# Optimization experiments

Hardware: AMD Instinct MI355X
Metric: run time of the kernel (lower is better)

The kernel has to match this reference:

```python
import jax, jax.numpy as jnp
import numpy as np

# Dims (see shape_source): resolution H must equal H_sp, W_sp must be 1 for the
# module's reshapes/broadcasts to be consistent.
B, HRES, WRES = 2, 4, 8192
H_SP, W_SP, H_SEC = 4, 1, 4          # window height, window width, sector height
C, NH = 512, 8
HD = C // NH
L = HRES * WRES                       # 32768 query tokens
NS = H_SEC * WRES                     # sector tokens (from k.view(B,C,H,W))
NW = B * (HRES // H_SP) * (WRES // W_SP)  # number of windows = B*WRES
SCALE = HD ** -0.5
EPS = 1e-5


def setup_inputs() -> dict:
    key = jax.random.key(0)
    ks = jax.random.split(key, 12)
    f32 = jnp.float32
    rn = lambda k, shp, s=1.0: jax.random.normal(k, shp, dtype=f32) * s
    return {
        "s": rn(ks[0], (B, NS, C)),
        "x": rn(ks[1], (B, L, C)),
        "s_pos": rn(ks[2], (B, H_SEC * W_SP, WRES // W_SP, 2)),
        "x_pos": rn(ks[3], (B, L, 2)),
        "Wq": rn(ks[4], (C, C), 0.02), "bq": jnp.zeros((C,), f32),
        "Wk": rn(ks[5], (C, C), 0.02), "bk": jnp.zeros((C,), f32),
        "Wv": rn(ks[6], (C, C), 0.02), "bv": jnp.zeros((C,), f32),
        "pw1": rn(ks[7], (16, 2), 0.3), "pb1": jnp.zeros((16,), f32),
        "bn_g": jnp.ones((16,), f32), "bn_b": jnp.zeros((16,), f32),
        "bn_m": jnp.zeros((16,), f32), "bn_v": jnp.ones((16,), f32),
        "pw2": rn(ks[8], (NH, 16), 0.3), "pb2": jnp.zeros((NH,), f32),
    }


def reference(s, x, s_pos, x_pos, Wq, bq, Wk, bk, Wv, bv,
              pw1, pb1, bn_g, bn_b, bn_m, bn_v, pw2, pb2):
    # ---- relative position bias (pointwise conv1d + BN(eval) + ReLU + conv1d) ----
    xp = x_pos.reshape(B, HRES // H_SP, H_SP, WRES // W_SP, W_SP, 2)
    xp = jnp.transpose(xp, (0, 1, 3, 5, 2, 4)).reshape(-1, 2, H_SP * W_SP)   # [NW,2,4]
    sp = jnp.transpose(s_pos, (0, 2, 3, 1)).reshape(-1, 2, H_SEC * W_SP)      # [NW,2,4]
    rel = xp[:, :, :, None] - sp[:, :, None, :]                               # [NW,2,4,4]
    rel = rel.reshape(NW, 2, -1)                                              # [NW,2,16]
    h = jnp.einsum('oc,ncl->nol', pw1, rel) + pb1[None, :, None]
    h = (h - bn_m[None, :, None]) * jax.lax.rsqrt(bn_v[None, :, None] + EPS)
    h = h * bn_g[None, :, None] + bn_b[None, :, None]
    h = jax.nn.relu(h)
    bias = jnp.einsum('oc,ncl->nol', pw2, h) + pb2[None, :, None]
    bias = bias.reshape(NW, NH, H_SP * W_SP, H_SEC * W_SP)                    # [NW,NH,4,4]

    # ---- q: im2cswin (true transpose to [B,C,H,W], then window partition) ----
    q = x @ Wq + bq                                                           # [B,L,C]
    q = jnp.transpose(q, (0, 2, 1)).reshape(B, C, HRES // H_SP, H_SP, WRES // W_SP, W_SP)
    q = jnp.transpose(q, (0, 2, 4, 3, 5, 1)).reshape(NW, H_SP * W_SP, NH, HD)
    q = jnp.transpose(q, (0, 2, 1, 3))                                        # [NW,NH,4,HD]

    # ---- k,v: raw view(B,C,H_sec,W) as in torch (memory reinterp, NOT transpose) ----
    def sector_windows(t):
        t = t.reshape(B, C, H_SEC, WRES)
        t = t.reshape(B, NH, HD, H_SEC, WRES // W_SP, W_SP)
        t = jnp.transpose(t, (0, 4, 1, 3, 5, 2))                              # [B,W,NH,Hs,Wsp,HD]
        return t.reshape(NW, NH, H_SEC * W_SP, HD)
    k = sector_windows(s @ Wk + bk)
    v = sector_windows(s @ Wv + bv)

    # ---- windowed attention with bias ----
    attn = jnp.einsum('nhqd,nhkd->nhqk', q * SCALE, k) + bias
    attn = jax.nn.softmax(attn, axis=-1)
    o = jnp.einsum('nhqk,nhkd->nhqd', attn, v)
    o = jnp.transpose(o, (0, 2, 1, 3)).reshape(NW, H_SP * W_SP, C)

    # ---- windows2img ----
    o = o.reshape(B, HRES // H_SP, WRES // W_SP, H_SP, W_SP, C)
    o = jnp.transpose(o, (0, 1, 3, 2, 4, 5)).reshape(B, L, C)
    return o
```

## Files before the change

kernel.cpp:

```cpp
#include <hip/hip_runtime.h>


typedef unsigned short u16;
typedef unsigned int u32;
typedef __attribute__((ext_vector_type(8))) short bf16x8;
typedef __attribute__((ext_vector_type(4))) float f32x4;
typedef __attribute__((ext_vector_type(8))) unsigned short u16x8;
typedef __attribute__((ext_vector_type(4))) unsigned short u16x4;
typedef __attribute__((ext_vector_type(4))) unsigned int u32x4;

__device__ __forceinline__ u16 f2b(float f) {
  u32 u = __float_as_uint(f);
  return (u16)((u + 0x7FFFu + ((u >> 16) & 1u)) >> 16);
}
__device__ __forceinline__ float b2f(u16 v) { return __uint_as_float(((u32)v) << 16); }
__device__ __forceinline__ float b2f_lo(u32 d) { return __uint_as_float(d << 16); }
__device__ __forceinline__ float b2f_hi(u32 d) { return __uint_as_float(d & 0xffff0000u); }
__device__ __forceinline__ u32 cvt_pk(float lo, float hi) {
  u32 r;
  asm("v_cvt_pk_bf16_f32 %0, %1, %2" : "=v"(r) : "v"(lo), "v"(hi));
  return r;
}
#define GLDS(g, l)                                                                     \
  __builtin_amdgcn_global_load_lds((const __attribute__((address_space(1))) void*)(g), \
                                   (__attribute__((address_space(3))) void*)(l), 16, 0, 0)
#define SBAR() __builtin_amdgcn_sched_barrier(0)

__global__ __launch_bounds__(256) void prep_kernel(
    const float* __restrict__ Wq, const float* __restrict__ Wk, const float* __restrict__ Wv,
    u16* __restrict__ Wt, const float* __restrict__ s, u16* __restrict__ sb,
    const float* __restrict__ xpos, const float* __restrict__ spos,
    const float* __restrict__ pw1, const float* __restrict__ pb1,
    const float* __restrict__ bng, const float* __restrict__ bnb,
    const float* __restrict__ bnm, const float* __restrict__ bnv,
    const float* __restrict__ pw2, const float* __restrict__ pb2, float* __restrict__ biasw) {
  int bid = (int)blockIdx.x;
  int t = threadIdx.x;
  if (bid < 16384) {
    size_t i = ((size_t)bid * 256 + t) * 8;
    float4 v0 = *(const float4*)(s + i);
    float4 v1 = *(const float4*)(s + i + 4);
    u32x4 pk;
    pk[0] = cvt_pk(v0.x, v0.y);
    pk[1] = cvt_pk(v0.z, v0.w);
    pk[2] = cvt_pk(v1.x, v1.y);
    pk[3] = cvt_pk(v1.z, v1.w);
    *(u32x4*)(sb + i) = pk;
  } else if (bid < 19456) {
    int r = bid - 16384;
    int mat = r >> 10, bx = r & 1023;
    const float* W = (mat == 0) ? Wq : (mat == 1) ? Wk : Wv;
    int g = bx * 256 + t;
    int n = g >> 9, k = g & 511;
    Wt[(size_t)mat * 262144 + g] = f2b(W[k * 512 + n]);
  } else {
    int bx = bid - 19456;
    int wl = t & 63, p = t >> 6;
    int n = bx * 64 + wl;
    int b = n >> 13, w = n & 8191;
    float Am[16], Bm[16], Cm[16];
#pragma unroll
    for (int m = 0; m < 16; ++m) {
      float scv = bng[m] * rsqrtf(bnv[m] + 1e-5f);
      Am[m] = pw1[2 * m] * scv;
      Bm[m] = pw1[2 * m + 1] * scv;
      Cm[m] = (pb1[m] - bnm[m]) * scv + bnb[m];
    }
    size_t xi = ((size_t)(b * 32768 + p * 8192 + w)) * 2;
    float xp0 = xpos[xi], xp1 = xpos[xi + 1];
#pragma unroll
    for (int ks = 0; ks < 4; ++ks) {
      size_t si = ((size_t)((b * 4 + ks) * 8192 + w)) * 2;
      float r0 = xp0 - spos[si];
      float r1 = xp1 - spos[si + 1];
      float o[8];
#pragma unroll
      for (int oo = 0; oo < 8; ++oo) o[oo] = pb2[oo];
#pragma unroll
      for (int m = 0; m < 16; ++m) {
        float h = fmaxf(Am[m] * r0 + Bm[m] * r1 + Cm[m], 0.f);
#pragma unroll
        for (int oo = 0; oo < 8; ++oo) o[oo] += pw2[oo * 16 + m] * h;
      }
#pragma unroll
      for (int oo = 0; oo < 8; ++oo)
        biasw[((size_t)(((b * 8 + oo) * 4 + p) * 4 + ks)) * 8192 + w] = o[oo];
    }
  }
}

__global__ __launch_bounds__(256, 3) void gemm_kernel(const float* __restrict__ A,
                                                      const u16* __restrict__ Bt,
                                                      const float* __restrict__ biasv,
                                                      u16* __restrict__ Out) {
  __shared__ u16 lds[24576];
  const int t = threadIdx.x, lane = t & 63, wv = t >> 6;
  const int id = (int)blockIdx.x;
  const int lg = (id & 7) * 256 + (id >> 3);
  const int mt = (lg >> 2) * 128, nt = (lg & 3) * 128;
  const int fr = lane & 15, kg = lane >> 4;
  const int wm = (wv & 1) * 64, wn = (wv >> 1) * 64;

  const int arow = lane >> 3;
  const int agr = (lane & 7) ^ arow;
  const int brow = lane >> 2;
  const int bgr = (lane & 3) ^ (brow & 3) ^ ((brow >> 2) & 3);

  const float* Abase = A + (size_t)mt * 512;
  const u16* Bbase = Bt + (size_t)nt * 512;

  f32x4 acc[4][4];
#pragma unroll
  for (int i = 0; i < 4; ++i)
#pragma unroll
    for (int j = 0; j < 4; ++j) acc[i][j] = (f32x4){0.f, 0.f, 0.f, 0.f};

#define STAGEQ(buf, kt)                                                       \
  {                                                                           \
    u16* Ab_ = lds + (buf)*8192;                                              \
    u16* Bb_ = lds + 16384 + (buf)*4096;                                      \
    _Pragma("unroll") for (int ii = 0; ii < 4; ++ii) {                        \
      int inst = wv * 4 + ii;                                                 \
      GLDS(Abase + (size_t)(inst * 8 + arow) * 512 + (kt) + agr * 4,          \
           Ab_ + inst * 512);                                                 \
    }                                                                         \
    _Pragma("unroll") for (int ii = 0; ii < 2; ++ii) {                        \
      int inst = wv * 2 + ii;                                                 \
      GLDS(Bbase + (size_t)(inst * 16 + brow) * 512 + (kt) + bgr * 8,         \
           Bb_ + inst * 512);                                                 \
    }                                                                         \
  }

  STAGEQ(0, 0);

  for (int ki = 0; ki < 16; ++ki) {
    int cur = ki & 1;
    if (ki < 15) {
      STAGEQ(cur ^ 1, (ki + 1) * 32);
      asm volatile("s_waitcnt vmcnt(6)" ::: "memory");
    } else {
      asm volatile("s_waitcnt vmcnt(0)" ::: "memory");
    }
    SBAR();
    __builtin_amdgcn_s_barrier();
    SBAR();

    const u16* Ab = lds + cur * 8192;
    const u16* Bb = lds + 16384 + cur * 4096;
    bf16x8 af[4], bfr[4];
#pragma unroll
    for (int i = 0; i < 4; ++i) {
      int r = wm + i * 16 + fr;
      int p0 = (2 * kg) ^ (r & 7), p1 = p0 ^ 1;
      f32x4 a0 = *(const f32x4*)&Ab[r * 64 + p0 * 8];
      f32x4 a1 = *(const f32x4*)&Ab[r * 64 + p1 * 8];
      union { bf16x8 v; u32 w[4]; } uu;
      uu.w[0] = cvt_pk(a0[0], a0[1]);
      uu.w[1] = cvt_pk(a0[2], a0[3]);
      uu.w[2] = cvt_pk(a1[0], a1[1]);
      uu.w[3] = cvt_pk(a1[2], a1[3]);
      af[i] = uu.v;
    }
#pragma unroll
    for (int j = 0; j < 4; ++j) {
      int r = wn + j * 16 + fr;
      int pos = kg ^ (r & 3) ^ ((r >> 2) & 3);
      bfr[j] = *(const bf16x8*)&Bb[r * 32 + pos * 8];
    }
    __builtin_amdgcn_s_setprio(1);
#pragma unroll
    for (int i = 0; i < 4; ++i)
#pragma unroll
      for (int j = 0; j < 4; ++j)
        acc[i][j] = __builtin_amdgcn_mfma_f32_16x16x32_bf16(af[i], bfr[j], acc[i][j], 0, 0, 0);
    __builtin_amdgcn_s_setprio(0);

    SBAR();
    __builtin_amdgcn_s_barrier();
    SBAR();
  }
#undef STAGEQ

  u16* Clds = lds;
#pragma unroll
  for (int i = 0; i < 4; ++i)
#pragma unroll
    for (int r = 0; r < 4; ++r) {
      int row = wm + i * 16 + kg * 4 + r;
#pragma unroll
      for (int j = 0; j < 4; ++j) {
        int ch = wn + j * 16 + fr;
        Clds[row * 136 + ch] = f2b(acc[i][j][r] + biasv[nt + ch]);
      }
    }
  __syncthreads();
#pragma unroll
  for (int c = 0; c < 8; ++c) {
    int off = c * 2048 + t * 8;
    int row = off >> 7, col = off & 127;
    *(u16x8*)(Out + (size_t)(mt + row) * 512 + nt + col) = *(const u16x8*)&Clds[row * 136 + col];
  }
}

__global__ __launch_bounds__(512, 4) void fused_attn_kernel(
    const u16* __restrict__ sb, const u16* __restrict__ WtK, const u16* __restrict__ WtV,
    const float* __restrict__ bK, const float* __restrict__ bV,
    const u16* __restrict__ Qt, const float* __restrict__ biasw, float* __restrict__ out) {
  __shared__ __align__(16) char LDS[74752];
  float* Xf = (float*)LDS;
  float* alds = (float*)(LDS + 4096);
  u16* Klds = (u16*)(LDS + 8192);
  u16* Vlds = (u16*)(LDS + 40960);

  const int t = threadIdx.x, lane = t & 63, wv = t >> 6;
  const int i0 = (int)blockIdx.x;
  const int xcd = i0 & 7, qq = i0 >> 3;
  const int g = (qq >> 6) * 8 + xcd, inner = qq & 63;
  const int b = g >> 4, u = g & 15;
  const int cg = inner >> 3, nh = inner & 7;
  const int fr = lane & 15, kg = lane >> 4;
  const int p3p = wv >> 1, dh = wv & 1;

  f32x4 accK[2][4], accV[2][4];
#pragma unroll
  for (int i = 0; i < 2; ++i)
#pragma unroll
    for (int j = 0; j < 4; ++j) {
      accK[i][j] = (f32x4){0.f, 0.f, 0.f, 0.f};
      accV[i][j] = (f32x4){0.f, 0.f, 0.f, 0.f};
    }

  const int lgr = (lane & 3) ^ ((lane >> 3) & 3);

#define STAGEF(buf, kt)                                                                 \
  {                                                                                     \
    u16* Sb_ = (u16*)(LDS) + (buf)*8192;                                                \
    _Pragma("unroll") for (int ii = 0; ii < 2; ++ii) {                                  \
      int i = wv * 2 + ii;                                                              \
      int r = i * 16 + (lane >> 2);                                                     \
      int grow = nh * 4096 + (r >> 2) * 64 + (r & 3) * 16 + u;                          \
      GLDS(sb + (size_t)(b * 32768 + grow) * 512 + (kt) + lgr * 8, Sb_ + i * 512);      \
    }                                                                                   \
    {                                                                                   \
      const u16* wsrc = (wv < 4) ? WtK : WtV;                                           \
      u16* Wb_ = (u16*)(LDS + 49152 + (buf)*8192 + ((wv < 4) ? 0 : 4096));              \
      int i = wv & 3;                                                                   \
      int r = i * 16 + (lane >> 2);                                                     \
      GLDS(wsrc + (size_t)(cg * 64 + r) * 512 + (kt) + lgr * 8, Wb_ + i * 512);         \
    }                                                                                   \
  }

  STAGEF(0, 0);
  STAGEF(1, 32);

  for (int ki = 0; ki < 16; ++ki) {
    int cur = ki % 3;
    if (ki < 15) {
      asm volatile("s_waitcnt vmcnt(3)" ::: "memory");
    } else {
      asm volatile("s_waitcnt vmcnt(0)" ::: "memory");
    }
    SBAR();
    __builtin_amdgcn_s_barrier();
    SBAR();

    const u16* Sb = (const u16*)(LDS) + cur * 8192;
    const u16* Kb = (const u16*)(LDS + 49152 + cur * 8192);
    const u16* Vb = (const u16*)(LDS + 49152 + cur * 8192 + 4096);
    bf16x8 af[2];
#pragma unroll
    for (int i = 0; i < 2; ++i) {
      int r = wv * 32 + i * 16 + fr;
      int gpos = kg ^ ((fr >> 1) & 3);
      af[i] = *(const bf16x8*)&Sb[r * 32 + gpos * 8];
    }
    {
      bf16x8 bkf[4];
#pragma unroll
      for (int j = 0; j < 4; ++j) {
        int r = j * 16 + fr;
        int gpos = kg ^ ((fr >> 1) & 3);
        bkf[j] = *(const bf16x8*)&Kb[r * 32 + gpos * 8];
      }
      __builtin_amdgcn_s_setprio(1);
#pragma unroll
      for (int i = 0; i < 2; ++i)
#pragma unroll
        for (int j = 0; j < 4; ++j)
          accK[i][j] = __builtin_amdgcn_mfma_f32_16x16x32_bf16(af[i], bkf[j], accK[i][j], 0, 0, 0);
      __builtin_amdgcn_s_setprio(0);
    }
    {
      bf16x8 bvf[4];
#pragma unroll
      for (int j = 0; j < 4; ++j) {
        int r = j * 16 + fr;
        int gpos = kg ^ ((fr >> 1) & 3);
        bvf[j] = *(const bf16x8*)&Vb[r * 32 + gpos * 8];
      }
      __builtin_amdgcn_s_setprio(1);
#pragma unroll
      for (int i = 0; i < 2; ++i)
#pragma unroll
        for (int j = 0; j < 4; ++j)
          accV[i][j] = __builtin_amdgcn_mfma_f32_16x16x32_bf16(af[i], bvf[j], accV[i][j], 0, 0, 0);
      __builtin_amdgcn_s_setprio(0);
    }
    SBAR();
    if (ki < 14) STAGEF((ki + 2) % 3, (ki + 2) * 32);
    SBAR();
  }
#undef STAGEF

  SBAR();
  float bkr[4], bvr[4];
#pragma unroll
  for (int j = 0; j < 4; ++j) {
    bkr[j] = bK[cg * 64 + j * 16 + fr];
    bvr[j] = bV[cg * 64 + j * 16 + fr];
  }
  u32x4 qv[4];
  {
    const u16* qp =
        Qt + (size_t)(b * 32768 + p3p * 8192 + u * 512 + cg * 64 + lane) * 512 + nh * 64 + dh * 32;
#pragma unroll
    for (int i = 0; i < 4; ++i) qv[i] = *(const u32x4*)(qp + i * 8);
  }
  float br[4];
  {
    const size_t bb = ((size_t)((b * 8 + nh) * 16 + p3p * 4)) * 8192 + u * 512 + cg * 64 + lane;
#pragma unroll
    for (int ks = 0; ks < 4; ++ks) br[ks] = biasw[bb + (size_t)ks * 8192];
  }
  SBAR();
  __builtin_amdgcn_s_barrier();
  SBAR();

#pragma unroll
  for (int i = 0; i < 2; ++i) {
    int d = wv * 8 + i * 4 + kg;
    int row0 = wv * 32 + i * 16 + kg * 4;
#pragma unroll
    for (int j = 0; j < 4; ++j) {
      int col = j * 16 + fr;
      u16x4 kq, vq;
#pragma unroll
      for (int rr = 0; rr < 4; ++rr) {
        kq[rr] = f2b(accK[i][j][rr] + bkr[j]);
        vq[rr] = f2b(accV[i][j][rr] + bvr[j]);
      }
      *(u16x4*)&Klds[(d * 64 + col) * 4] = kq;
      *(u16x4*)&Vlds[col * 264 + row0] = vq;
    }
  }
  __syncthreads();

  float sc[4] = {0.f, 0.f, 0.f, 0.f};
#pragma unroll
  for (int dd = 0; dd < 32; ++dd) {
    int d = dh * 32 + dd;
    u32 word = qv[dd >> 3][(dd >> 1) & 3];
    float qd = (dd & 1) ? b2f_hi(word) : b2f_lo(word);
    u16x4 kv4 = *(const u16x4*)&Klds[(d * 64 + lane) * 4];
#pragma unroll
    for (int ks = 0; ks < 4; ++ks) sc[ks] += qd * b2f(kv4[ks]);
  }
  if (dh == 1) {
#pragma unroll
    for (int ks = 0; ks < 4; ++ks) Xf[(p3p * 4 + ks) * 64 + lane] = sc[ks];
  }
  __syncthreads();

  if (dh == 0) {
    float sv[4];
#pragma unroll
    for (int ks = 0; ks < 4; ++ks)
      sv[ks] = (sc[ks] + Xf[(p3p * 4 + ks) * 64 + lane]) * 0.125f + br[ks];
    float mx = fmaxf(fmaxf(sv[0], sv[1]), fmaxf(sv[2], sv[3]));
    float e0 = __expf(sv[0] - mx), e1 = __expf(sv[1] - mx), e2 = __expf(sv[2] - mx),
          e3 = __expf(sv[3] - mx);
    float inv = 1.f / (e0 + e1 + e2 + e3);
#pragma unroll
    for (int ks = 0; ks < 4; ++ks) {
      float e = (ks == 0) ? e0 : (ks == 1) ? e1 : (ks == 2) ? e2 : e3;
      alds[(p3p * 4 + ks) * 64 + lane] = e * inv;
    }
  }
  __syncthreads();

  float* ob = out + (size_t)(b * 32768 + p3p * 8192 + u * 512 + cg * 64) * 512 + nh * 64 + lane;
#pragma unroll
  for (int cc = 0; cc < 32; ++cc) {
    int c = dh * 32 + cc;
    u16x4 vvv = *(const u16x4*)&Vlds[c * 264 + lane * 4];
    float a0 = alds[(p3p * 4 + 0) * 64 + c];
    float a1 = alds[(p3p * 4 + 1) * 64 + c];
    float a2 = alds[(p3p * 4 + 2) * 64 + c];
    float a3 = alds[(p3p * 4 + 3) * 64 + c];
    float o = a0 * b2f(vvv[0]) + a1 * b2f(vvv[1]) + a2 * b2f(vvv[2]) + a3 * b2f(vvv[3]);
    ob[(size_t)c * 512] = o;
  }
}

extern "C" void kernel_launch(void* const* d_in, const int* in_sizes, int n_in,
                              void* d_out, int out_size, void* d_ws, size_t ws_size,
                              hipStream_t stream) {
  (void)in_sizes; (void)n_in; (void)out_size; (void)ws_size;
  const float* s     = (const float*)d_in[0];
  const float* x     = (const float*)d_in[1];
  const float* s_pos = (const float*)d_in[2];
  const float* x_pos = (const float*)d_in[3];
  const float* Wq = (const float*)d_in[4];  const float* bq = (const float*)d_in[5];
  const float* Wk = (const float*)d_in[6];  const float* bk = (const float*)d_in[7];
  const float* Wv = (const float*)d_in[8];  const float* bv = (const float*)d_in[9];
  const float* pw1 = (const float*)d_in[10]; const float* pb1 = (const float*)d_in[11];
  const float* bng = (const float*)d_in[12]; const float* bnb = (const float*)d_in[13];
  const float* bnm = (const float*)d_in[14]; const float* bnv = (const float*)d_in[15];
  const float* pw2 = (const float*)d_in[16]; const float* pb2 = (const float*)d_in[17];
  float* out = (float*)d_out;

  char* ws = (char*)d_ws;
  u16* Qt = (u16*)ws;
  float* biasw = (float*)(ws + 67108864);
  u16* Wt = (u16*)(ws + 75497472);
  u16* sbuf = (u16*)(ws + 77070336);

  prep_kernel<<<dim3(19712), 256, 0, stream>>>(Wq, Wk, Wv, Wt, s, sbuf, x_pos, s_pos, pw1, pb1,
                                               bng, bnb, bnm, bnv, pw2, pb2, biasw);
  gemm_kernel<<<dim3(2048), 256, 0, stream>>>(x, Wt, bq, Qt);
  fused_attn_kernel<<<dim3(2048), 512, 0, stream>>>(sbuf, Wt + 262144, Wt + 524288, bk, bv,
                                                    Qt, biasw, out);
}
```

Before: 237.1 us.

## Load GEMM A operand directly to registers and retile fused K/V projection waves

The Q-projection GEMM no longer stages the fp32 A tile through LDS. Each lane loads its own rows straight from global memory into registers and converts them to bf16. This shrinks LDS use and raises the occupancy hint from 3 to 4 blocks, but gives up coalesced LDS staging and exposes global load latency inside the loop. The fused attention kernel's K/V projection now uses a 4x2 MFMA tile per wave instead of 2x4, which changes how many A and B fragments each wave reads from LDS.

```diff
diff --git a/kernel.cpp b/kernel.cpp
--- a/kernel.cpp
+++ b/kernel.cpp
@@ -89,11 +89,13 @@
   }
 }
 
-__global__ __launch_bounds__(256, 3) void gemm_kernel(const float* __restrict__ A,
+__global__ __launch_bounds__(256, 4) void gemm_kernel(const float* __restrict__ A,
                                                       const u16* __restrict__ Bt,
                                                       const float* __restrict__ biasv,
                                                       u16* __restrict__ Out) {
-  __shared__ u16 lds[24576];
+  __shared__ __align__(16) char LDSC[34816];
+  u16* Blds = (u16*)LDSC;
+  u16* Clds = (u16*)LDSC;
   const int t = threadIdx.x, lane = t & 63, wv = t >> 6;
   const int id = (int)blockIdx.x;
   const int lg = (id & 7) * 256 + (id >> 3);
@@ -101,12 +103,10 @@
   const int fr = lane & 15, kg = lane >> 4;
   const int wm = (wv & 1) * 64, wn = (wv >> 1) * 64;
 
-  const int arow = lane >> 3;
-  const int agr = (lane & 7) ^ arow;
   const int brow = lane >> 2;
   const int bgr = (lane & 3) ^ (brow & 3) ^ ((brow >> 2) & 3);
 
-  const float* Abase = A + (size_t)mt * 512;
+  const float* Abase = A + (size_t)(mt + wm + fr) * 512 + kg * 8;
   const u16* Bbase = Bt + (size_t)nt * 512;
 
   f32x4 acc[4][4];
@@ -115,15 +115,9 @@
 #pragma unroll
     for (int j = 0; j < 4; ++j) acc[i][j] = (f32x4){0.f, 0.f, 0.f, 0.f};
 
-#define STAGEQ(buf, kt)                                                       \
+#define STAGEB(buf, kt)                                                       \
   {                                                                           \
-    u16* Ab_ = lds + (buf)*8192;                                              \
-    u16* Bb_ = lds + 16384 + (buf)*4096;                                      \
-    _Pragma("unroll") for (int ii = 0; ii < 4; ++ii) {                        \
-      int inst = wv * 4 + ii;                                                 \
-      GLDS(Abase + (size_t)(inst * 8 + arow) * 512 + (kt) + agr * 4,          \
-           Ab_ + inst * 512);                                                 \
-    }                                                                         \
+    u16* Bb_ = Blds + (buf)*4096;                                             \
     _Pragma("unroll") for (int ii = 0; ii < 2; ++ii) {                        \
       int inst = wv * 2 + ii;                                                 \
       GLDS(Bbase + (size_t)(inst * 16 + brow) * 512 + (kt) + bgr * 8,         \
@@ -131,13 +125,21 @@
     }                                                                         \
   }
 
-  STAGEQ(0, 0);
+  STAGEB(0, 0);
 
   for (int ki = 0; ki < 16; ++ki) {
     int cur = ki & 1;
+    f32x4 a0[4], a1[4];
+#pragma unroll
+    for (int i = 0; i < 4; ++i) {
+      const float* ap = Abase + (size_t)(i * 16) * 512 + ki * 32;
+      a0[i] = *(const f32x4*)ap;
+      a1[i] = *(const f32x4*)(ap + 4);
+    }
+    SBAR();
     if (ki < 15) {
-      STAGEQ(cur ^ 1, (ki + 1) * 32);
-      asm volatile("s_waitcnt vmcnt(6)" ::: "memory");
+      STAGEB(cur ^ 1, (ki + 1) * 32);
+      asm volatile("s_waitcnt vmcnt(2)" ::: "memory");
     } else {
       asm volatile("s_waitcnt vmcnt(0)" ::: "memory");
     }
@@ -145,22 +147,17 @@
     __builtin_amdgcn_s_barrier();
     SBAR();
 
-    const u16* Ab = lds + cur * 8192;
-    const u16* Bb = lds + 16384 + cur * 4096;
     bf16x8 af[4], bfr[4];
 #pragma unroll
     for (int i = 0; i < 4; ++i) {
-      int r = wm + i * 16 + fr;
-      int p0 = (2 * kg) ^ (r & 7), p1 = p0 ^ 1;
-      f32x4 a0 = *(const f32x4*)&Ab[r * 64 + p0 * 8];
-      f32x4 a1 = *(const f32x4*)&Ab[r * 64 + p1 * 8];
       union { bf16x8 v; u32 w[4]; } uu;
-      uu.w[0] = cvt_pk(a0[0], a0[1]);
-      uu.w[1] = cvt_pk(a0[2], a0[3]);
-      uu.w[2] = cvt_pk(a1[0], a1[1]);
-      uu.w[3] = cvt_pk(a1[2], a1[3]);
+      uu.w[0] = cvt_pk(a0[i][0], a0[i][1]);
+      uu.w[1] = cvt_pk(a0[i][2], a0[i][3]);
+      uu.w[2] = cvt_pk(a1[i][0], a1[i][1]);
+      uu.w[3] = cvt_pk(a1[i][2], a1[i][3]);
       af[i] = uu.v;
     }
+    const u16* Bb = Blds + cur * 4096;
 #pragma unroll
     for (int j = 0; j < 4; ++j) {
       int r = wn + j * 16 + fr;
@@ -179,9 +176,8 @@
     __builtin_amdgcn_s_barrier();
     SBAR();
   }
-#undef STAGEQ
-
-  u16* Clds = lds;
+#undef STAGEB
+
 #pragma unroll
   for (int i = 0; i < 4; ++i)
 #pragma unroll
@@ -220,12 +216,13 @@
   const int cg = inner >> 3, nh = inner & 7;
   const int fr = lane & 15, kg = lane >> 4;
   const int p3p = wv >> 1, dh = wv & 1;
-
-  f32x4 accK[2][4], accV[2][4];
-#pragma unroll
-  for (int i = 0; i < 2; ++i)
-#pragma unroll
-    for (int j = 0; j < 4; ++j) {
+  const int mg = wv >> 1, ng = wv & 1;
+
+  f32x4 accK[4][2], accV[4][2];
+#pragma unroll
+  for (int i = 0; i < 4; ++i)
+#pragma unroll
+    for (int j = 0; j < 2; ++j) {
       accK[i][j] = (f32x4){0.f, 0.f, 0.f, 0.f};
       accV[i][j] = (f32x4){0.f, 0.f, 0.f, 0.f};
     }
@@ -267,42 +264,42 @@
     const u16* Sb = (const u16*)(LDS) + cur * 8192;
     const u16* Kb = (const u16*)(LDS + 49152 + cur * 8192);
     const u16* Vb = (const u16*)(LDS + 49152 + cur * 8192 + 4096);
-    bf16x8 af[2];
-#pragma unroll
-    for (int i = 0; i < 2; ++i) {
-      int r = wv * 32 + i * 16 + fr;
+    bf16x8 af[4];
+#pragma unroll
+    for (int i = 0; i < 4; ++i) {
+      int r = mg * 64 + i * 16 + fr;
       int gpos = kg ^ ((fr >> 1) & 3);
       af[i] = *(const bf16x8*)&Sb[r * 32 + gpos * 8];
     }
     {
-      bf16x8 bkf[4];
-#pragma unroll
-      for (int j = 0; j < 4; ++j) {
-        int r = j * 16 + fr;
+      bf16x8 bkf[2];
+#pragma unroll
+      for (int j = 0; j < 2; ++j) {
+        int r = ng * 32 + j * 16 + fr;
         int gpos = kg ^ ((fr >> 1) & 3);
         bkf[j] = *(const bf16x8*)&Kb[r * 32 + gpos * 8];
       }
       __builtin_amdgcn_s_setprio(1);
 #pragma unroll
-      for (int i = 0; i < 2; ++i)
-#pragma unroll
-        for (int j = 0; j < 4; ++j)
+      for (int i = 0; i < 4; ++i)
+#pragma unroll
+        for (int j = 0; j < 2; ++j)
           accK[i][j] = __builtin_amdgcn_mfma_f32_16x16x32_bf16(af[i], bkf[j], accK[i][j], 0, 0, 0);
       __builtin_amdgcn_s_setprio(0);
     }
     {
-      bf16x8 bvf[4];
-#pragma unroll
-      for (int j = 0; j < 4; ++j) {
-        int r = j * 16 + fr;
+      bf16x8 bvf[2];
+#pragma unroll
+      for (int j = 0; j < 2; ++j) {
+        int r = ng * 32 + j * 16 + fr;
         int gpos = kg ^ ((fr >> 1) & 3);
         bvf[j] = *(const bf16x8*)&Vb[r * 32 + gpos * 8];
       }
       __builtin_amdgcn_s_setprio(1);
 #pragma unroll
-      for (int i = 0; i < 2; ++i)
-#pragma unroll
-        for (int j = 0; j < 4; ++j)
+      for (int i = 0; i < 4; ++i)
+#pragma unroll
+        for (int j = 0; j < 2; ++j)
           accV[i][j] = __builtin_amdgcn_mfma_f32_16x16x32_bf16(af[i], bvf[j], accV[i][j], 0, 0, 0);
       __builtin_amdgcn_s_setprio(0);
     }
@@ -313,11 +310,11 @@
 #undef STAGEF
 
   SBAR();
-  float bkr[4], bvr[4];
-#pragma unroll
-  for (int j = 0; j < 4; ++j) {
-    bkr[j] = bK[cg * 64 + j * 16 + fr];
-    bvr[j] = bV[cg * 64 + j * 16 + fr];
+  float bkr[2], bvr[2];
+#pragma unroll
+  for (int j = 0; j < 2; ++j) {
+    bkr[j] = bK[cg * 64 + ng * 32 + j * 16 + fr];
+    bvr[j] = bV[cg * 64 + ng * 32 + j * 16 + fr];
   }
   u32x4 qv[4];
   {
@@ -337,12 +334,12 @@
   SBAR();
 
 #pragma unroll
-  for (int i = 0; i < 2; ++i) {
-    int d = wv * 8 + i * 4 + kg;
-    int row0 = wv * 32 + i * 16 + kg * 4;
-#pragma unroll
-    for (int j = 0; j < 4; ++j) {
-      int col = j * 16 + fr;
+  for (int i = 0; i < 4; ++i) {
+    int d = mg * 16 + i * 4 + kg;
+    int row0 = mg * 64 + i * 16 + kg * 4;
+#pragma unroll
+    for (int j = 0; j < 2; ++j) {
+      int col = ng * 32 + j * 16 + fr;
       u16x4 kq, vq;
 #pragma unroll
       for (int rr = 0; rr < 4; ++rr) {
```

New measurement: 304.1 us. 1.28x slower.
